# Performance work log

Hardware: AMD Instinct MI355X
Metric: run time of the kernel (lower is better)

## Reference

```python
import jax, jax.numpy as jnp
import numpy as np

V, D, DU, H = 50000, 256, 1024, 128
TEMP = 0.01

def time_cosine_emb(t, d_model):
    half = d_model // 2
    div_term = jnp.exp(jnp.arange(half, dtype=jnp.float32) * (-np.log(10000.0) / half))
    scaled = t[..., None] * div_term  # (B, L, half)
    return jnp.concatenate([jnp.sin(scaled), jnp.cos(scaled)], axis=-1)

def setup_inputs() -> dict:
    key = jax.random.key(0)
    ks = jax.random.split(key, 12)
    B, L = 64, 2048
    q_seq = jax.random.randint(ks[0], (B, L), 0, V)
    r_seq = jax.random.randint(ks[1], (B, L), 0, 3)
    t_seq = jax.random.uniform(ks[2], (B, L), dtype=jnp.float32) * 1000.0
    mask = jnp.ones((B, L), dtype=jnp.float32)
    q_tab = jax.random.normal(ks[3], (V, D), dtype=jnp.float32) * 0.02
    q_tab = q_tab.at[0].set(0.0)  # padding_idx=0
    r_tab = jax.random.normal(ks[4], (3, D), dtype=jnp.float32) * 0.02
    r_tab = r_tab.at[0].set(0.0)  # padding_idx=0
    virtual_node = jax.random.normal(ks[5], (1, D), dtype=jnp.float32)
    Ws1 = jax.random.normal(ks[6], (H, 2 * D), dtype=jnp.float32) * (1.0 / np.sqrt(2 * D))
    bs1 = jnp.zeros((H,), dtype=jnp.float32)
    Ws2 = jax.random.normal(ks[7], (1, H), dtype=jnp.float32) * (1.0 / np.sqrt(H))
    bs2 = jnp.zeros((1,), dtype=jnp.float32)
    Wa = jax.random.normal(ks[8], (DU, D), dtype=jnp.float32) * (1.0 / np.sqrt(D))
    ba = jnp.zeros((DU,), dtype=jnp.float32)
    return {"q_seq": q_seq, "r_seq": r_seq, "t_seq": t_seq, "mask": mask,
            "q_tab": q_tab, "r_tab": r_tab, "virtual_node": virtual_node,
            "Ws1": Ws1, "bs1": bs1, "Ws2": Ws2, "bs2": bs2, "Wa": Wa, "ba": ba}

def reference(q_seq, r_seq, t_seq, mask, q_tab, r_tab, virtual_node, Ws1, bs1, Ws2, bs2, Wa, ba):
    B, L = q_seq.shape
    d_model = q_tab.shape[1]
    # embedding gathers + trig time embedding
    h_events = q_tab[q_seq] + r_tab[r_seq] + time_cosine_emb(t_seq, d_model)  # (B,L,D)
    h_virtual = jnp.broadcast_to(virtual_node[None, :, :], (B, L, d_model))
    pair = jnp.concatenate([h_events, h_virtual], axis=-1)  # (B,L,2D)
    # struct_head: Linear -> LeakyReLU(0.2) -> Linear
    hdn = jax.nn.leaky_relu(jnp.einsum('bld,hd->blh', pair, Ws1) + bs1, 0.2)
    logits = jnp.einsum('blh,oh->blo', hdn, Ws2) + bs2  # (B,L,1)
    A_hat = jax.nn.sigmoid(logits / TEMP) * mask[..., None]
    # aggregator: Linear -> LeakyReLU(0.2)
    h_trans = jax.nn.leaky_relu(jnp.einsum('bld,ud->blu', h_events, Wa) + ba, 0.2)  # (B,L,DU)
    u_i = jnp.sum(h_trans * A_hat, axis=1)  # (B,DU)
    return (u_i, jnp.squeeze(A_hat, -1))
```

## Files before the change

### kernel.cpp

```cpp
#include <hip/hip_runtime.h>

typedef unsigned short ushort_t;
typedef unsigned int uint_t;

typedef short bf16x8 __attribute__((ext_vector_type(8)));
typedef float f32x4 __attribute__((ext_vector_type(4)));

#define MFMA16(a, b, c) __builtin_amdgcn_mfma_f32_16x16x32_bf16(a, b, c, 0, 0, 0)

__device__ __forceinline__ ushort_t f2bf(float f) {
    uint_t u = __float_as_uint(f);
    u += 0x7fffu + ((u >> 16) & 1u);
    return (ushort_t)(u >> 16);
}
__device__ __forceinline__ float bf2f(ushort_t h) {
    return __uint_as_float(((uint_t)h) << 16);
}

__global__ void k_prep(const float* __restrict__ Ws1, const float* __restrict__ bs1,
                       const float* __restrict__ virt, const float* __restrict__ Wa,
                       float* __restrict__ consth, ushort_t* __restrict__ wa_b,
                       ushort_t* __restrict__ ws1h, ushort_t* __restrict__ ws1l,
                       float* __restrict__ u_i) {
    int b = blockIdx.x;
    if (b < 8) {
        int w = threadIdx.x >> 6, lane = threadIdx.x & 63;
#pragma unroll
        for (int i = 0; i < 4; ++i) {
            int row = b * 16 + w * 4 + i;
            const float* rp = Ws1 + row * 512 + 256;
            float4 v = *(const float4*)(rp + lane * 4);
            float4 vv = *(const float4*)(virt + lane * 4);
            float s = v.x * vv.x + v.y * vv.y + v.z * vv.z + v.w * vv.w;
            s += __shfl_xor(s, 1, 64);
            s += __shfl_xor(s, 2, 64);
            s += __shfl_xor(s, 4, 64);
            s += __shfl_xor(s, 8, 64);
            s += __shfl_xor(s, 16, 64);
            s += __shfl_xor(s, 32, 64);
            if (lane == 0) consth[row] = bs1[row] + s;
        }
        return;
    }
    if (b >= 152) {
        int t = (b - 152) * 1024 + threadIdx.x * 4;
        float4 z = {0.f, 0.f, 0.f, 0.f};
        *(float4*)(u_i + t) = z;
        return;
    }
    const float* src;
    int src_stride, tid;
    ushort_t *dhi, *dlo;
    if (b <= 135) {
        tid = (b - 8) * 256 + threadIdx.x;
        src = Wa; src_stride = 256; dhi = wa_b; dlo = nullptr;
    } else {
        tid = (b - 136) * 256 + threadIdx.x;
        src = Ws1; src_stride = 512; dhi = ws1h; dlo = ws1l;
    }
    int pl = tid & 15, kc = (tid >> 4) & 31, pt = tid >> 9;
    int row = pt * 16 + pl;
    const float* s = src + (size_t)row * src_stride + kc * 8;
    ushort_t hs[8], ls[8];
#pragma unroll
    for (int j = 0; j < 8; ++j) {
        float v = s[j];
        ushort_t h = f2bf(v);
        hs[j] = h;
        ls[j] = f2bf(v - bf2f(h));
    }
    uint4 hv;
    hv.x = hs[0] | ((uint_t)hs[1] << 16); hv.y = hs[2] | ((uint_t)hs[3] << 16);
    hv.z = hs[4] | ((uint_t)hs[5] << 16); hv.w = hs[6] | ((uint_t)hs[7] << 16);
    *(uint4*)(dhi + (size_t)tid * 8) = hv;
    if (dlo) {
        uint4 lv;
        lv.x = ls[0] | ((uint_t)ls[1] << 16); lv.y = ls[2] | ((uint_t)ls[3] << 16);
        lv.z = ls[4] | ((uint_t)ls[5] << 16); lv.w = ls[6] | ((uint_t)ls[7] << 16);
        *(uint4*)(dlo + (size_t)tid * 8) = lv;
    }
}

__global__ __launch_bounds__(256, 2) void k_embed(
    const int* __restrict__ q_seq, const int* __restrict__ r_seq,
    const float* __restrict__ t_seq, const float* __restrict__ q_tab,
    const float* __restrict__ r_tab,
    const ushort_t* __restrict__ ws1h, const ushort_t* __restrict__ ws1l,
    const float* __restrict__ consth, const float* __restrict__ Ws2,
    const float* __restrict__ bs2, const float* __restrict__ mask,
    float* __restrict__ out_ahat, ushort_t* __restrict__ ghi) {
    __shared__ __align__(16) ushort_t sAhi[16384];
    __shared__ __align__(16) ushort_t sAlo[8192];
    __shared__ float sdiv[128];
    __shared__ float sLogit[64];
    int tid = threadIdx.x;
    if (tid < 128) sdiv[tid] = __expf((float)tid * -0.07195578415606394f);
    if (tid < 64) sLogit[tid] = 0.0f;
    int w = tid >> 6, lane = tid & 63;
    int pl = lane & 15, kq = lane >> 4;
    int nl = pl;
    int p0 = blockIdx.x * 64;
    int p = p0 + w * 16 + pl;
    int qv = q_seq[p];
    int rr = r_seq[p];
    float tt = t_seq[p];
    const float* grow = q_tab + (size_t)qv * 256;
    const float* rrow = r_tab + (size_t)rr * 256;
    uint4* gdst = (uint4*)(ghi + (size_t)blockIdx.x * 16384);
    __syncthreads();
    uint4 lo_hold[4];
#pragma unroll
    for (int it = 0; it < 8; ++it) {
        int kc = it * 4 + kq;
        int k0 = kc * 8;
        float4 qa = *(const float4*)(grow + kc * 8);
        float4 qb = *(const float4*)(grow + kc * 8 + 4);
        float4 ra = *(const float4*)(rrow + kc * 8);
        float4 rb = *(const float4*)(rrow + kc * 8 + 4);
        float v[8] = {qa.x + ra.x, qa.y + ra.y, qa.z + ra.z, qa.w + ra.w,
                      qb.x + rb.x, qb.y + rb.y, qb.z + rb.z, qb.w + rb.w};
        bool iscos = (kc >= 16);
#pragma unroll
        for (int j = 0; j < 8; ++j) {
            float ang = tt * sdiv[(k0 + j) & 127];
            v[j] += iscos ? __cosf(ang) : __sinf(ang);
        }
        ushort_t hs[8], ls[8];
#pragma unroll
        for (int j = 0; j < 8; ++j) {
            ushort_t h = f2bf(v[j]);
            hs[j] = h;
            ls[j] = (ushort_t)(__float_as_uint(v[j] - bf2f(h)) >> 16);
        }
        uint4 hv, lv;
        hv.x = hs[0] | ((uint_t)hs[1] << 16); hv.y = hs[2] | ((uint_t)hs[3] << 16);
        hv.z = hs[4] | ((uint_t)hs[5] << 16); hv.w = hs[6] | ((uint_t)hs[7] << 16);
        lv.x = ls[0] | ((uint_t)ls[1] << 16); lv.y = ls[2] | ((uint_t)ls[3] << 16);
        lv.z = ls[4] | ((uint_t)ls[5] << 16); lv.w = ls[6] | ((uint_t)ls[7] << 16);
        int unit = (w * 32 + kc) * 16 + pl;
        *(uint4*)(sAhi + unit * 8) = hv;
        gdst[unit] = hv;
        if (it < 4) {
            *(uint4*)(sAlo + ((w * 16 + kc) * 16 + pl) * 8) = lv;
        } else {
            lo_hold[it - 4] = lv;
        }
    }
    __syncthreads();
    {
        f32x4 acc[4][2];
        f32x4 z4 = {0.f, 0.f, 0.f, 0.f};
#pragma unroll
        for (int mt = 0; mt < 4; ++mt)
#pragma unroll
            for (int nt = 0; nt < 2; ++nt) acc[mt][nt] = z4;
#pragma unroll
        for (int ks = 0; ks < 8; ++ks) {
            if (ks == 4) {
                __syncthreads();
#pragma unroll
                for (int it = 4; it < 8; ++it) {
                    int kc = it * 4 + kq;
                    *(uint4*)(sAlo + ((w * 16 + (kc - 16)) * 16 + pl) * 8) = lo_hold[it - 4];
                }
                __syncthreads();
            }
            bf16x8 bh[2], bl[2];
#pragma unroll
            for (int nt = 0; nt < 2; ++nt) {
                int off = (((w * 2 + nt) * 32 + ks * 4 + kq) * 16 + nl) * 8;
                bh[nt] = *(const bf16x8*)(ws1h + off);
                bl[nt] = *(const bf16x8*)(ws1l + off);
            }
#pragma unroll
            for (int mth = 0; mth < 2; ++mth) {
                bf16x8 ahi[2], alo[2];
#pragma unroll
                for (int mi = 0; mi < 2; ++mi) {
                    int mt = mth * 2 + mi;
                    ahi[mi] = *(const bf16x8*)&sAhi[((mt * 32 + ks * 4 + kq) * 16 + nl) * 8];
                    alo[mi] = *(const bf16x8*)&sAlo[((mt * 16 + (ks & 3) * 4 + kq) * 16 + nl) * 8];
                }
#pragma unroll
                for (int mi = 0; mi < 2; ++mi)
#pragma unroll
                    for (int nt = 0; nt < 2; ++nt) {
                        int mt = mth * 2 + mi;
                        acc[mt][nt] = MFMA16(ahi[mi], bh[nt], acc[mt][nt]);
                        acc[mt][nt] = MFMA16(alo[mi], bh[nt], acc[mt][nt]);
                        acc[mt][nt] = MFMA16(ahi[mi], bl[nt], acc[mt][nt]);
                    }
            }
        }
        float ps[4][4];
#pragma unroll
        for (int mt = 0; mt < 4; ++mt)
#pragma unroll
            for (int r = 0; r < 4; ++r) ps[mt][r] = 0.f;
#pragma unroll
        for (int nt = 0; nt < 2; ++nt) {
            int ng = w * 32 + nt * 16 + nl;
            float chv = consth[ng], w2 = Ws2[ng];
#pragma unroll
            for (int mt = 0; mt < 4; ++mt)
#pragma unroll
                for (int r = 0; r < 4; ++r) {
                    float v = acc[mt][nt][r] + chv;
                    v = fmaxf(v, 0.2f * v);
                    ps[mt][r] += v * w2;
                }
        }
#pragma unroll
        for (int mt = 0; mt < 4; ++mt)
#pragma unroll
            for (int r = 0; r < 4; ++r) {
                float x = ps[mt][r];
                x += __shfl_xor(x, 1, 64);
                x += __shfl_xor(x, 2, 64);
                x += __shfl_xor(x, 4, 64);
                x += __shfl_xor(x, 8, 64);
                ps[mt][r] = x;
            }
        if (nl == 0) {
#pragma unroll
            for (int mt = 0; mt < 4; ++mt)
#pragma unroll
                for (int r = 0; r < 4; ++r)
                    atomicAdd(&sLogit[mt * 16 + kq * 4 + r], ps[mt][r]);
        }
    }
    __syncthreads();
    if (tid < 64) {
        int pp = p0 + tid;
        float lg = sLogit[tid] + bs2[0];
        float y = lg * 100.0f;
        y = fminf(fmaxf(y, -60.f), 60.f);
        float a = 1.0f / (1.0f + expf(-y));
        out_ahat[pp] = a * mask[pp];
    }
}

__global__ __launch_bounds__(256, 2) void k_wa(
    const ushort_t* __restrict__ ghi, const float* __restrict__ out_ahat,
    const ushort_t* __restrict__ wa_b, const float* __restrict__ ba,
    float* __restrict__ u_i) {
    __shared__ __align__(16) ushort_t sA[16384];
    __shared__ float sAh[64];
    int tid = threadIdx.x;
    int p0 = blockIdx.x * 64;
    {
        const uint4* src = (const uint4*)(ghi + (size_t)blockIdx.x * 16384);
        uint4* dst = (uint4*)sA;
#pragma unroll
        for (int i = 0; i < 8; ++i) dst[tid + i * 256] = src[tid + i * 256];
    }
    if (tid < 64) sAh[tid] = out_ahat[p0 + tid];
    __syncthreads();
    int w = tid >> 6, lane = tid & 63;
    int pl = lane & 15, kq = lane >> 4;
    int nl = pl;
    float ah[16];
#pragma unroll
    for (int mt = 0; mt < 4; ++mt)
#pragma unroll
        for (int r = 0; r < 4; ++r) ah[mt * 4 + r] = sAh[mt * 16 + kq * 4 + r];
    int bidx = p0 >> 11;
#pragma unroll 1
    for (int nblk = 0; nblk < 4; ++nblk) {
#pragma unroll 1
        for (int hf = 0; hf < 2; ++hf) {
            const ushort_t* gB = wa_b + (size_t)(w * 16 + nblk * 4 + hf * 2) * 4096 + lane * 8;
            f32x4 acc[4][2];
            bf16x8 bfr[2][2];
#pragma unroll
            for (int nt = 0; nt < 2; ++nt)
                bfr[0][nt] = *(const bf16x8*)(gB + nt * 4096);
#pragma unroll
            for (int ks = 0; ks < 8; ++ks) {
                int cur = ks & 1, nxt = cur ^ 1;
                if (ks < 7) {
#pragma unroll
                    for (int nt = 0; nt < 2; ++nt)
                        bfr[nxt][nt] = *(const bf16x8*)(gB + nt * 4096 + (ks + 1) * 512);
                }
                bf16x8 a_[4];
#pragma unroll
                for (int mt = 0; mt < 4; ++mt)
                    a_[mt] = *(const bf16x8*)&sA[((mt * 32 + ks * 4 + kq) * 16 + nl) * 8];
                if (ks == 0) {
                    f32x4 z4 = {0.f, 0.f, 0.f, 0.f};
#pragma unroll
                    for (int mt = 0; mt < 4; ++mt)
#pragma unroll
                        for (int nt = 0; nt < 2; ++nt)
                            acc[mt][nt] = MFMA16(a_[mt], bfr[0][nt], z4);
                } else {
#pragma unroll
                    for (int mt = 0; mt < 4; ++mt)
#pragma unroll
                        for (int nt = 0; nt < 2; ++nt)
                            acc[mt][nt] = MFMA16(a_[mt], bfr[cur][nt], acc[mt][nt]);
                }
            }
#pragma unroll
            for (int nt = 0; nt < 2; ++nt) {
                int ng = w * 256 + nblk * 64 + (hf * 2 + nt) * 16 + nl;
                float ban = ba[ng];
                float s = 0.f;
#pragma unroll
                for (int mt = 0; mt < 4; ++mt)
#pragma unroll
                    for (int r = 0; r < 4; ++r) {
                        float v = acc[mt][nt][r] + ban;
                        v = fmaxf(v, 0.2f * v);
                        s += v * ah[mt * 4 + r];
                    }
                s += __shfl_xor(s, 16, 64);
                s += __shfl_xor(s, 32, 64);
                if (kq == 0) atomicAdd(&u_i[bidx * 1024 + ng], s);
            }
        }
    }
}

__global__ __launch_bounds__(256, 2) void k_fused_fb(
    const int* __restrict__ q_seq, const int* __restrict__ r_seq,
    const float* __restrict__ t_seq, const float* __restrict__ q_tab,
    const float* __restrict__ r_tab,
    const ushort_t* __restrict__ ws1h, const ushort_t* __restrict__ ws1l,
    const float* __restrict__ consth, const float* __restrict__ Ws2,
    const float* __restrict__ bs2, const float* __restrict__ mask,
    const ushort_t* __restrict__ wa_b, const float* __restrict__ ba,
    float* __restrict__ out_ahat, float* __restrict__ u_i) {
    __shared__ __align__(16) ushort_t sAhi[16384];
    __shared__ __align__(16) ushort_t sAlo[16384];
    __shared__ float sdiv[128];
    __shared__ float sLogit[64];
    __shared__ float sAh[64];
    int tid = threadIdx.x;
    if (tid < 128) sdiv[tid] = __expf((float)tid * -0.07195578415606394f);
    if (tid < 64) sLogit[tid] = 0.0f;
    int w = tid >> 6, lane = tid & 63;
    int pl = lane & 15, kq = lane >> 4;
    int nl = pl;
    int p0 = blockIdx.x * 64;
    int p = p0 + w * 16 + pl;
    int qv = q_seq[p];
    int rr = r_seq[p];
    float tt = t_seq[p];
    const float* grow = q_tab + (size_t)qv * 256;
    const float* rrow = r_tab + (size_t)rr * 256;
    __syncthreads();
#pragma unroll
    for (int it = 0; it < 8; ++it) {
        int kc = it * 4 + kq;
        int k0 = kc * 8;
        float4 qa = *(const float4*)(grow + kc * 8);
        float4 qb = *(const float4*)(grow + kc * 8 + 4);
        float4 ra = *(const float4*)(rrow + kc * 8);
        float4 rb = *(const float4*)(rrow + kc * 8 + 4);
        float v[8] = {qa.x + ra.x, qa.y + ra.y, qa.z + ra.z, qa.w + ra.w,
                      qb.x + rb.x, qb.y + rb.y, qb.z + rb.z, qb.w + rb.w};
        bool iscos = (kc >= 16);
#pragma unroll
        for (int j = 0; j < 8; ++j) {
            float ang = tt * sdiv[(k0 + j) & 127];
            v[j] += iscos ? __cosf(ang) : __sinf(ang);
        }
        ushort_t hs[8], ls[8];
#pragma unroll
        for (int j = 0; j < 8; ++j) {
            ushort_t h = f2bf(v[j]);
            hs[j] = h;
            ls[j] = (ushort_t)(__float_as_uint(v[j] - bf2f(h)) >> 16);
        }
        uint4 hv, lv;
        hv.x = hs[0] | ((uint_t)hs[1] << 16); hv.y = hs[2] | ((uint_t)hs[3] << 16);
        hv.z = hs[4] | ((uint_t)hs[5] << 16); hv.w = hs[6] | ((uint_t)hs[7] << 16);
        lv.x = ls[0] | ((uint_t)ls[1] << 16); lv.y = ls[2] | ((uint_t)ls[3] << 16);
        lv.z = ls[4] | ((uint_t)ls[5] << 16); lv.w = ls[6] | ((uint_t)ls[7] << 16);
        int loff = ((w * 32 + kc) * 16 + pl) * 8;
        *(uint4*)(sAhi + loff) = hv;
        *(uint4*)(sAlo + loff) = lv;
    }
    __syncthreads();
    {
        f32x4 acc[4][2];
        f32x4 z4 = {0.f, 0.f, 0.f, 0.f};
#pragma unroll
        for (int mt = 0; mt < 4; ++mt)
#pragma unroll
            for (int nt = 0; nt < 2; ++nt) acc[mt][nt] = z4;
        bf16x8 bh[2][2], bl[2][2];
#pragma unroll
        for (int nt = 0; nt < 2; ++nt) {
            int off = (((w * 2 + nt) * 32 + kq) * 16 + nl) * 8;
            bh[0][nt] = *(const bf16x8*)(ws1h + off);
            bl[0][nt] = *(const bf16x8*)(ws1l + off);
        }
#pragma unroll
        for (int ks = 0; ks < 8; ++ks) {
            int cur = ks & 1, nxt = cur ^ 1;
            if (ks < 7) {
#pragma unroll
                for (int nt = 0; nt < 2; ++nt) {
                    int off = (((w * 2 + nt) * 32 + (ks + 1) * 4 + kq) * 16 + nl) * 8;
                    bh[nxt][nt] = *(const bf16x8*)(ws1h + off);
                    bl[nxt][nt] = *(const bf16x8*)(ws1l + off);
                }
            }
            bf16x8 ahi[4], alo[4];
#pragma unroll
            for (int mt = 0; mt < 4; ++mt) {
                int off = ((mt * 32 + ks * 4 + kq) * 16 + nl) * 8;
                ahi[mt] = *(const bf16x8*)&sAhi[off];
                alo[mt] = *(const bf16x8*)&sAlo[off];
            }
#pragma unroll
            for (int mt = 0; mt < 4; ++mt)
#pragma unroll
                for (int nt = 0; nt < 2; ++nt) {
                    acc[mt][nt] = MFMA16(ahi[mt], bh[cur][nt], acc[mt][nt]);
                    acc[mt][nt] = MFMA16(alo[mt], bh[cur][nt], acc[mt][nt]);
                    acc[mt][nt] = MFMA16(ahi[mt], bl[cur][nt], acc[mt][nt]);
                }
        }
        float ps[4][4];
#pragma unroll
        for (int mt = 0; mt < 4; ++mt)
#pragma unroll
            for (int r = 0; r < 4; ++r) ps[mt][r] = 0.f;
#pragma unroll
        for (int nt = 0; nt < 2; ++nt) {
            int ng = w * 32 + nt * 16 + nl;
            float chv = consth[ng], w2 = Ws2[ng];
#pragma unroll
            for (int mt = 0; mt < 4; ++mt)
#pragma unroll
                for (int r = 0; r < 4; ++r) {
                    float v = acc[mt][nt][r] + chv;
                    v = fmaxf(v, 0.2f * v);
                    ps[mt][r] += v * w2;
                }
        }
#pragma unroll
        for (int mt = 0; mt < 4; ++mt)
#pragma unroll
            for (int r = 0; r < 4; ++r) {
                float x = ps[mt][r];
                x += __shfl_xor(x, 1, 64);
                x += __shfl_xor(x, 2, 64);
                x += __shfl_xor(x, 4, 64);
                x += __shfl_xor(x, 8, 64);
                ps[mt][r] = x;
            }
        if (nl == 0) {
#pragma unroll
            for (int mt = 0; mt < 4; ++mt)
#pragma unroll
                for (int r = 0; r < 4; ++r)
                    atomicAdd(&sLogit[mt * 16 + kq * 4 + r], ps[mt][r]);
        }
    }
    __syncthreads();
    if (tid < 64) {
        int pp = p0 + tid;
        float lg = sLogit[tid] + bs2[0];
        float y = lg * 100.0f;
        y = fminf(fmaxf(y, -60.f), 60.f);
        float a = 1.0f / (1.0f + expf(-y));
        float av = a * mask[pp];
        out_ahat[pp] = av;
        sAh[tid] = av;
    }
    __syncthreads();
    {
        float ah[16];
#pragma unroll
        for (int mt = 0; mt < 4; ++mt)
#pragma unroll
            for (int r = 0; r < 4; ++r) ah[mt * 4 + r] = sAh[mt * 16 + kq * 4 + r];
        int bidx = p0 >> 11;
#pragma unroll 1
        for (int nblk = 0; nblk < 4; ++nblk) {
#pragma unroll 1
            for (int hf = 0; hf < 2; ++hf) {
                const ushort_t* gB = wa_b + (size_t)(w * 16 + nblk * 4 + hf * 2) * 4096 + lane * 8;
                f32x4 acc[4][2];
                bf16x8 bfr[2][2];
#pragma unroll
                for (int nt = 0; nt < 2; ++nt)
                    bfr[0][nt] = *(const bf16x8*)(gB + nt * 4096);
#pragma unroll
                for (int ks = 0; ks < 8; ++ks) {
                    int cur = ks & 1, nxt = cur ^ 1;
                    if (ks < 7) {
#pragma unroll
                        for (int nt = 0; nt < 2; ++nt)
                            bfr[nxt][nt] = *(const bf16x8*)(gB + nt * 4096 + (ks + 1) * 512);
                    }
                    bf16x8 a_[4];
#pragma unroll
                    for (int mt = 0; mt < 4; ++mt)
                        a_[mt] = *(const bf16x8*)&sAhi[((mt * 32 + ks * 4 + kq) * 16 + nl) * 8];
                    if (ks == 0) {
                        f32x4 z4 = {0.f, 0.f, 0.f, 0.f};
#pragma unroll
                        for (int mt = 0; mt < 4; ++mt)
#pragma unroll
                            for (int nt = 0; nt < 2; ++nt)
                                acc[mt][nt] = MFMA16(a_[mt], bfr[0][nt], z4);
                    } else {
#pragma unroll
                        for (int mt = 0; mt < 4; ++mt)
#pragma unroll
                            for (int nt = 0; nt < 2; ++nt)
                                acc[mt][nt] = MFMA16(a_[mt], bfr[cur][nt], acc[mt][nt]);
                    }
                }
#pragma unroll
                for (int nt = 0; nt < 2; ++nt) {
                    int ng = w * 256 + nblk * 64 + (hf * 2 + nt) * 16 + nl;
                    float ban = ba[ng];
                    float s = 0.f;
#pragma unroll
                    for (int mt = 0; mt < 4; ++mt)
#pragma unroll
                        for (int r = 0; r < 4; ++r) {
                            float v = acc[mt][nt][r] + ban;
                            v = fmaxf(v, 0.2f * v);
                            s += v * ah[mt * 4 + r];
                        }
                    s += __shfl_xor(s, 16, 64);
                    s += __shfl_xor(s, 32, 64);
                    if (kq == 0) atomicAdd(&u_i[bidx * 1024 + ng], s);
                }
            }
        }
    }
}

extern "C" void kernel_launch(void* const* d_in, const int* in_sizes, int n_in,
                              void* d_out, int out_size, void* d_ws, size_t ws_size,
                              hipStream_t stream) {
    const int* q_seq = (const int*)d_in[0];
    const int* r_seq = (const int*)d_in[1];
    const float* t_seq = (const float*)d_in[2];
    const float* mask = (const float*)d_in[3];
    const float* q_tab = (const float*)d_in[4];
    const float* r_tab = (const float*)d_in[5];
    const float* virt = (const float*)d_in[6];
    const float* Ws1 = (const float*)d_in[7];
    const float* bs1 = (const float*)d_in[8];
    const float* Ws2 = (const float*)d_in[9];
    const float* bs2 = (const float*)d_in[10];
    const float* Wa = (const float*)d_in[11];
    const float* ba = (const float*)d_in[12];
    float* out = (float*)d_out;

    ushort_t* wa_b = (ushort_t*)d_ws;
    ushort_t* ws1h = wa_b + 262144;
    ushort_t* ws1l = ws1h + 32768;
    float* ch = (float*)(ws1l + 32768);
    ushort_t* ghi = (ushort_t*)(ch + 128);
    const size_t need = 524288 + 65536 + 65536 + 512 + 67108864;

    hipLaunchKernelGGL(k_prep, dim3(216), dim3(256), 0, stream,
                       Ws1, bs1, virt, Wa, ch, wa_b, ws1h, ws1l, out);
    if (ws_size >= need) {
        hipLaunchKernelGGL(k_embed, dim3(2048), dim3(256), 0, stream,
                           q_seq, r_seq, t_seq, q_tab, r_tab, ws1h, ws1l, ch, Ws2,
                           bs2, mask, out + 65536, ghi);
        hipLaunchKernelGGL(k_wa, dim3(2048), dim3(256), 0, stream,
                           ghi, out + 65536, wa_b, ba, out);
    } else {
        hipLaunchKernelGGL(k_fused_fb, dim3(2048), dim3(256), 0, stream,
                           q_seq, r_seq, t_seq, q_tab, r_tab, ws1h, ws1l, ch, Ws2,
                           bs2, mask, wa_b, ba, out + 65536, out);
    }
}
```

Baseline: 239.8 us.

## Restructure k_wa to keep Wa slice in LDS and stream activations

Rewrites the Wa aggregator GEMM kernel so that each block stages a 128-column slice of the bf16 Wa weights in shared memory and streams 512 positions of activations from global memory, instead of staging 64 positions of activations and streaming all of Wa from global. Partial weighted sums are kept in registers across the 8 position chunks, so atomics to u_i happen once per block instead of once per chunk. The grid layout changes to slice-major indexing, and LDS use grows to 64KB per block, which may limit occupancy. The activation fragments are now read with a different indexing pattern, which implicitly assumes a particular layout of ghi.

Measured after the change: 289.3 us. +20.6%, slower.

```diff
diff --git a/kernel.cpp b/kernel.cpp
--- a/kernel.cpp
+++ b/kernel.cpp
@@ -244,81 +244,92 @@
     const ushort_t* __restrict__ ghi, const float* __restrict__ out_ahat,
     const ushort_t* __restrict__ wa_b, const float* __restrict__ ba,
     float* __restrict__ u_i) {
-    __shared__ __align__(16) ushort_t sA[16384];
-    __shared__ float sAh[64];
+    __shared__ __align__(16) ushort_t sB[32768];
+    __shared__ float sAh[512];
     int tid = threadIdx.x;
-    int p0 = blockIdx.x * 64;
+    int nslice = blockIdx.x >> 8;
+    int pblk = blockIdx.x & 255;
+    int P0 = pblk * 512;
     {
-        const uint4* src = (const uint4*)(ghi + (size_t)blockIdx.x * 16384);
-        uint4* dst = (uint4*)sA;
-#pragma unroll
-        for (int i = 0; i < 8; ++i) dst[tid + i * 256] = src[tid + i * 256];
-    }
-    if (tid < 64) sAh[tid] = out_ahat[p0 + tid];
+        const uint4* src = (const uint4*)(wa_b + (size_t)nslice * 32768);
+        uint4* dst = (uint4*)sB;
+#pragma unroll
+        for (int i = 0; i < 16; ++i) dst[tid + i * 256] = src[tid + i * 256];
+    }
+    sAh[tid] = out_ahat[P0 + tid];
+    sAh[tid + 256] = out_ahat[P0 + tid + 256];
     __syncthreads();
     int w = tid >> 6, lane = tid & 63;
-    int pl = lane & 15, kq = lane >> 4;
-    int nl = pl;
-    float ah[16];
-#pragma unroll
-    for (int mt = 0; mt < 4; ++mt)
-#pragma unroll
-        for (int r = 0; r < 4; ++r) ah[mt * 4 + r] = sAh[mt * 16 + kq * 4 + r];
-    int bidx = p0 >> 11;
+    int kq = lane >> 4, nl = lane & 15;
+    float ban[2];
+#pragma unroll
+    for (int nt = 0; nt < 2; ++nt)
+        ban[nt] = ba[nslice * 128 + w * 32 + nt * 16 + nl];
+    float s_nt[2] = {0.f, 0.f};
 #pragma unroll 1
-    for (int nblk = 0; nblk < 4; ++nblk) {
-#pragma unroll 1
-        for (int hf = 0; hf < 2; ++hf) {
-            const ushort_t* gB = wa_b + (size_t)(w * 16 + nblk * 4 + hf * 2) * 4096 + lane * 8;
-            f32x4 acc[4][2];
-            bf16x8 bfr[2][2];
+    for (int c = 0; c < 8; ++c) {
+        const ushort_t* gA = ghi + ((size_t)(pblk * 8 + c)) * 16384 + lane * 8;
+        f32x4 acc[4][2];
+        bf16x8 afr[2][4];
+#pragma unroll
+        for (int mt = 0; mt < 4; ++mt)
+            afr[0][mt] = *(const bf16x8*)(gA + mt * 4096);
+#pragma unroll
+        for (int ks = 0; ks < 8; ++ks) {
+            int cur = ks & 1, nxt = cur ^ 1;
+            if (ks < 7) {
+#pragma unroll
+                for (int mt = 0; mt < 4; ++mt)
+                    afr[nxt][mt] = *(const bf16x8*)(gA + mt * 4096 + (ks + 1) * 512);
+            }
+            bf16x8 b_[2];
 #pragma unroll
             for (int nt = 0; nt < 2; ++nt)
-                bfr[0][nt] = *(const bf16x8*)(gB + nt * 4096);
-#pragma unroll
-            for (int ks = 0; ks < 8; ++ks) {
-                int cur = ks & 1, nxt = cur ^ 1;
-                if (ks < 7) {
+                b_[nt] = *(const bf16x8*)&sB[(w * 2 + nt) * 4096 + ks * 512 + lane * 8];
+            if (ks == 0) {
+                f32x4 z4 = {0.f, 0.f, 0.f, 0.f};
+#pragma unroll
+                for (int mt = 0; mt < 4; ++mt)
 #pragma unroll
                     for (int nt = 0; nt < 2; ++nt)
-                        bfr[nxt][nt] = *(const bf16x8*)(gB + nt * 4096 + (ks + 1) * 512);
-                }
-                bf16x8 a_[4];
+                        acc[mt][nt] = MFMA16(afr[0][mt], b_[nt], z4);
+            } else {
 #pragma unroll
                 for (int mt = 0; mt < 4; ++mt)
-                    a_[mt] = *(const bf16x8*)&sA[((mt * 32 + ks * 4 + kq) * 16 + nl) * 8];
-                if (ks == 0) {
-                    f32x4 z4 = {0.f, 0.f, 0.f, 0.f};
-#pragma unroll
-                    for (int mt = 0; mt < 4; ++mt)
-#pragma unroll
-                        for (int nt = 0; nt < 2; ++nt)
-                            acc[mt][nt] = MFMA16(a_[mt], bfr[0][nt], z4);
-                } else {
-#pragma unroll
-                    for (int mt = 0; mt < 4; ++mt)
-#pragma unroll
-                        for (int nt = 0; nt < 2; ++nt)
-                            acc[mt][nt] = MFMA16(a_[mt], bfr[cur][nt], acc[mt][nt]);
-                }
-            }
-#pragma unroll
-            for (int nt = 0; nt < 2; ++nt) {
-                int ng = w * 256 + nblk * 64 + (hf * 2 + nt) * 16 + nl;
-                float ban = ba[ng];
-                float s = 0.f;
-#pragma unroll
-                for (int mt = 0; mt < 4; ++mt)
-#pragma unroll
-                    for (int r = 0; r < 4; ++r) {
-                        float v = acc[mt][nt][r] + ban;
-                        v = fmaxf(v, 0.2f * v);
-                        s += v * ah[mt * 4 + r];
-                    }
-                s += __shfl_xor(s, 16, 64);
-                s += __shfl_xor(s, 32, 64);
-                if (kq == 0) atomicAdd(&u_i[bidx * 1024 + ng], s);
-            }
+#pragma unroll
+                    for (int nt = 0; nt < 2; ++nt)
+                        acc[mt][nt] = MFMA16(afr[cur][mt], b_[nt], acc[mt][nt]);
+            }
+        }
+        float ah[16];
+#pragma unroll
+        for (int mt = 0; mt < 4; ++mt)
+#pragma unroll
+            for (int r = 0; r < 4; ++r)
+                ah[mt * 4 + r] = sAh[c * 64 + mt * 16 + kq * 4 + r];
+#pragma unroll
+        for (int nt = 0; nt < 2; ++nt) {
+            float s = 0.f;
+#pragma unroll
+            for (int mt = 0; mt < 4; ++mt)
+#pragma unroll
+                for (int r = 0; r < 4; ++r) {
+                    float v = acc[mt][nt][r] + ban[nt];
+                    v = fmaxf(v, 0.2f * v);
+                    s += v * ah[mt * 4 + r];
+                }
+            s_nt[nt] += s;
+        }
+    }
+    int seq = P0 >> 11;
+#pragma unroll
+    for (int nt = 0; nt < 2; ++nt) {
+        float s = s_nt[nt];
+        s += __shfl_xor(s, 16, 64);
+        s += __shfl_xor(s, 32, 64);
+        if (kq == 0) {
+            int ng = nslice * 128 + w * 32 + nt * 16 + nl;
+            atomicAdd(&u_i[seq * 1024 + ng], s);
         }
     }
 }
```
